# Performance work log

Measured on AMD Instinct MI355X. Metric: run time of the kernel, lower is better.

## Reference

```python
import jax, jax.numpy as jnp
import numpy as np

B, S, D, H = 2, 2048, 1024, 16
HD = D // H          # head_dim = 64
HALF = HD // 2       # rotary pair count = 32


def rope_freqs(seq_len, half, base=10000.0):
    # Llama-style: theta_j = base^(-2j/head_dim), angle m*theta_j
    inv = 1.0 / (base ** (np.arange(0, half, dtype=np.float32) / half))
    ang = np.arange(seq_len, dtype=np.float32)[:, None] * inv[None, :]  # [S, half]
    return jnp.asarray(np.cos(ang)), jnp.asarray(np.sin(ang))


def setup_inputs() -> dict:
    key = jax.random.key(0)
    kx, kq, kk, kv, ko = jax.random.split(key, 5)
    cos, sin = rope_freqs(S, HALF)  # real/imag of m_theta_polar_tensor
    s = 0.02
    return {
        "x": jax.random.normal(kx, (B, S, D), dtype=jnp.float32),
        "freqs_cos": cos,
        "freqs_sin": sin,
        "Wq": jax.random.normal(kq, (D, D), dtype=jnp.float32) * s,
        "Wk": jax.random.normal(kk, (D, D), dtype=jnp.float32) * s,
        "Wv": jax.random.normal(kv, (D, D), dtype=jnp.float32) * s,
        "Wout": jax.random.normal(ko, (D, D), dtype=jnp.float32) * s,
    }


def _apply_rope(t, cos, sin):
    # t: [B, S, H, HD]; rotate consecutive pairs (complex multiply)
    b, s, h, hd = t.shape
    tr = t.reshape(b, s, h, hd // 2, 2)
    t0, t1 = tr[..., 0], tr[..., 1]
    c = cos[None, :, None, :]  # [1, S, 1, HALF]
    sn = sin[None, :, None, :]
    o0 = t0 * c - t1 * sn
    o1 = t0 * sn + t1 * c
    return jnp.stack([o0, o1], axis=-1).reshape(b, s, h, hd)


def reference(x, freqs_cos, freqs_sin, Wq, Wk, Wv, Wout):
    b, s, _ = x.shape
    q = (x @ Wq).reshape(b, s, H, HD)
    k = (x @ Wk).reshape(b, s, H, HD)
    v = (x @ Wv).reshape(b, s, H, HD)
    q = _apply_rope(q, freqs_cos, freqs_sin)
    k = _apply_rope(k, freqs_cos, freqs_sin)
    # [B, H, S, S]
    scores = jnp.einsum("bqhd,bkhd->bhqk", q, k) / jnp.sqrt(jnp.float32(HD))
    causal = jnp.triu(jnp.ones((s, s), dtype=bool), k=1)
    scores = jnp.where(causal[None, None], -jnp.inf, scores)
    weights = jax.nn.softmax(scores, axis=-1)
    vectors = jnp.einsum("bhqk,bkhd->bqhd", weights, v).reshape(b, s, D)
    return vectors @ Wout
```

## Files before the change

kernel.cpp:

```cpp
#include <hip/hip_runtime.h>
#include <stdint.h>

typedef unsigned short u16;
typedef __attribute__((ext_vector_type(8))) short short8;
typedef __attribute__((ext_vector_type(4))) float f32x4;
typedef __attribute__((ext_vector_type(4))) unsigned short ushort4v;
typedef __attribute__((ext_vector_type(2))) unsigned int uint2v;

#define NB 2
#define NS 2048
#define ND 1024
#define NH 16
#define HDIM 64
#define NHALF 32
#define QSCALE 0.18033688f
#define NEGBIG -3.0e38f

__device__ __forceinline__ float bf2f(u16 u) {
  union { unsigned u; float f; } v; v.u = ((unsigned)u) << 16; return v.f;
}
__device__ __forceinline__ u16 f2bf(float f) {
  union { float f; unsigned u; } v; v.f = f;
  unsigned r = v.u + 0x7fffu + ((v.u >> 16) & 1u);
  return (u16)(r >> 16);
}

__device__ __forceinline__ unsigned cvt_pk_bf16(float lo, float hi) {
  unsigned r;
  asm("v_cvt_pk_bf16_f32 %0, %1, %2" : "=v"(r) : "v"(lo), "v"(hi));
  return r;
}

__device__ __forceinline__ void gld_lds16(const u16* g, u16* l) {
  void* gv = (void*)g;
  __builtin_amdgcn_global_load_lds((__attribute__((address_space(1))) void*)gv,
                                   (__attribute__((address_space(3))) void*)l, 16, 0, 0);
}

__global__ void prep(const float* __restrict__ x, u16* __restrict__ xb,
                     const float* __restrict__ W0, const float* __restrict__ W1,
                     const float* __restrict__ W2, const float* __restrict__ W3,
                     u16* __restrict__ dqkv, u16* __restrict__ dout) {
  __shared__ float tile[32][33];
  const int bid = blockIdx.x;
  if (bid < 4096) {
    int i = bid * 256 + threadIdx.x;
    float4 v = ((const float4*)x)[i];
    ushort4v o;
    o.x = f2bf(v.x); o.y = f2bf(v.y); o.z = f2bf(v.z); o.w = f2bf(v.w);
    ((ushort4v*)xb)[i] = o;
  } else {
    int idx = bid - 4096;
    const int z = idx >> 10;
    idx &= 1023;
    const int bx = idx & 31, by = idx >> 5;
    const float* W = (z == 0) ? W0 : (z == 1) ? W1 : (z == 2) ? W2 : W3;
    u16* dst = (z < 3) ? (dqkv + (size_t)z * ND * ND) : dout;
    const int n0 = bx * 32, k0 = by * 32;
    const int tx = threadIdx.x & 31, ty = threadIdx.x >> 5;
#pragma unroll
    for (int i = 0; i < 4; ++i)
      tile[ty + i * 8][tx] = W[(size_t)(k0 + ty + i * 8) * ND + n0 + tx];
    __syncthreads();
#pragma unroll
    for (int i = 0; i < 4; ++i)
      dst[(size_t)(n0 + ty + i * 8) * ND + k0 + tx] = f2bf(tile[tx][ty + i * 8]);
  }
}

template<int MI, int MODE>
__device__ __forceinline__ void gemm_body(
    u16* smem0, int bx, int by,
    const u16* __restrict__ A, const u16* __restrict__ BT,
    u16* __restrict__ qo, u16* __restrict__ ko, u16* __restrict__ vo,
    float* __restrict__ fo,
    const float* __restrict__ cosT, const float* __restrict__ sinT) {
  constexpr int BUFSZ = MI * 2048 + 8192;
  const int tid = threadIdx.x;
  const int w = tid >> 6, lane = tid & 63;
  const int lr = lane & 15, lg = lane >> 4;
  const int bm = by * (MI * 32), bn = bx << 7;
  const int wr = (w >> 1) * (MI * 16), wc = (w & 1) << 6;
  f32x4 acc[MI][4] = {};

  const int arow = tid >> 3;
  const int aslot = (tid & 7) ^ (arow & 7);
  const u16* ags = A + (size_t)(bm + arow) * ND + (aslot << 3);
  const u16* bgs = BT + (size_t)(bn + arow) * ND + (aslot << 3);

  int af_off[MI][2], bf_off[4][2];
#pragma unroll
  for (int mi = 0; mi < MI; ++mi)
#pragma unroll
    for (int kk = 0; kk < 2; ++kk)
      af_off[mi][kk] = (wr + mi * 16 + lr) * 64 + ((((kk << 2) + lg) ^ (lr & 7)) << 3);
#pragma unroll
  for (int ni = 0; ni < 4; ++ni)
#pragma unroll
    for (int kk = 0; kk < 2; ++kk)
      bf_off[ni][kk] = (wc + ni * 16 + lr) * 64 + ((((kk << 2) + lg) ^ (lr & 7)) << 3);

  auto stage = [&](int buf, int kt) {
    u16* dst = smem0 + buf * BUFSZ;
#pragma unroll
    for (int it = 0; it < MI; ++it)
      gld_lds16(ags + it * (32 * ND) + kt, dst + it * 2048 + w * 512);
#pragma unroll
    for (int it = 0; it < 4; ++it)
      gld_lds16(bgs + it * (32 * ND) + kt, dst + MI * 2048 + it * 2048 + w * 512);
  };

  stage(0, 0);
  __syncthreads();
  int cur = 0;
  for (int kt = 0; kt < ND; kt += 64) {
    if (kt + 64 < ND) stage(cur ^ 1, kt + 64);
    const u16* As = smem0 + cur * BUFSZ;
    const u16* Bs = As + MI * 2048;
#pragma unroll
    for (int kk = 0; kk < 2; ++kk) {
      short8 af[MI], bfr[4];
#pragma unroll
      for (int mi = 0; mi < MI; ++mi)
        af[mi] = *(const short8*)(As + af_off[mi][kk]);
#pragma unroll
      for (int ni = 0; ni < 4; ++ni)
        bfr[ni] = *(const short8*)(Bs + bf_off[ni][kk]);
#pragma unroll
      for (int mi = 0; mi < MI; ++mi)
#pragma unroll
        for (int ni = 0; ni < 4; ++ni) {
          if (MODE == 0)
            acc[mi][ni] = __builtin_amdgcn_mfma_f32_16x16x32_bf16(bfr[ni], af[mi], acc[mi][ni], 0, 0, 0);
          else
            acc[mi][ni] = __builtin_amdgcn_mfma_f32_16x16x32_bf16(af[mi], bfr[ni], acc[mi][ni], 0, 0, 0);
        }
    }
    __syncthreads();
    cur ^= 1;
  }

  if (MODE == 0) {
#pragma unroll
    for (int mi = 0; mi < MI; ++mi) {
      const int m = bm + wr + mi * 16 + lr;
      const int b = m >> 11, s = m & 2047;
      const float* cbase = cosT + s * NHALF;
      const float* sbase = sinT + s * NHALF;
#pragma unroll
      for (int ni = 0; ni < 4; ++ni) {
        const int n = bn + wc + ni * 16 + (lg << 2);
        const int which = n >> 10, hh = (n >> 6) & 15, d0 = n & 63;
        u16* dst = which == 0 ? qo : ko;
        const float sc = which == 0 ? QSCALE : 1.0f;
        const float2 cp = *(const float2*)(cbase + (d0 >> 1));
        const float2 sp = *(const float2*)(sbase + (d0 >> 1));
        const float v0 = acc[mi][ni][0], v1 = acc[mi][ni][1];
        const float v2 = acc[mi][ni][2], v3 = acc[mi][ni][3];
        uint2v pk;
        pk.x = cvt_pk_bf16((v0 * cp.x - v1 * sp.x) * sc, (v0 * sp.x + v1 * cp.x) * sc);
        pk.y = cvt_pk_bf16((v2 * cp.y - v3 * sp.y) * sc, (v2 * sp.y + v3 * cp.y) * sc);
        *(uint2v*)(dst + (((size_t)(b * NH + hh) * NS + s) << 6) + d0) = pk;
      }
    }
  } else if (MODE == 1) {
#pragma unroll
    for (int mi = 0; mi < MI; ++mi) {
#pragma unroll
      for (int ni = 0; ni < 4; ++ni) {
        const int n = bn + wc + ni * 16 + lr;
        const int hh = n >> 6, d = n & 63;
        const int m0 = bm + wr + mi * 16 + (lg << 2);
        const int b = m0 >> 11, s0 = m0 & 2047;
        uint2v pk;
        pk.x = cvt_pk_bf16(acc[mi][ni][0], acc[mi][ni][1]);
        pk.y = cvt_pk_bf16(acc[mi][ni][2], acc[mi][ni][3]);
        *(uint2v*)(vo + ((size_t)(b * NH + hh) * HDIM + d) * NS + s0) = pk;
      }
    }
  } else {
#pragma unroll
    for (int mi = 0; mi < MI; ++mi)
#pragma unroll
      for (int ni = 0; ni < 4; ++ni)
#pragma unroll
        for (int j = 0; j < 4; ++j) {
          const int m = bm + wr + mi * 16 + (lg << 2) + j;
          const int n = bn + wc + ni * 16 + lr;
          fo[(size_t)m * ND + n] = acc[mi][ni][j];
        }
  }
}

__global__ __launch_bounds__(256) void gemm_qkv(
    const u16* __restrict__ xb, const u16* __restrict__ WTqkv, const u16* __restrict__ WTv,
    u16* __restrict__ Qb, u16* __restrict__ Kb, u16* __restrict__ VT,
    const float* __restrict__ fc, const float* __restrict__ fs) {
  __shared__ u16 smem[2 * 16384];
  const int bid = blockIdx.x;
  if (bid < 512) {
    gemm_body<4, 0>(smem, bid & 15, bid >> 4, xb, WTqkv, Qb, Kb, nullptr, nullptr, fc, fs);
  } else {
    const int idx = bid - 512;
    gemm_body<2, 1>(smem, idx & 7, idx >> 3, xb, WTv, nullptr, nullptr, VT, nullptr, nullptr, nullptr);
  }
}

__global__ __launch_bounds__(256) void gemm_out_k(
    const u16* __restrict__ Ob, const u16* __restrict__ WTo, float* __restrict__ out) {
  __shared__ u16 smem[2 * 12288];
  gemm_body<2, 2>(smem, blockIdx.x, blockIdx.y, Ob, WTo, nullptr, nullptr, nullptr, out, nullptr, nullptr);
}

__global__ __launch_bounds__(512) void attn_k(
    const u16* __restrict__ Qb, const u16* __restrict__ Kb,
    const u16* __restrict__ VT, u16* __restrict__ Ob) {
  __shared__ u16 K2[2][4096];
  __shared__ u16 V2[2][4096];
  __shared__ u16 Pl[8][1024];
  const int tid = threadIdx.x, w = tid >> 6, lane = tid & 63;
  const int lr = lane & 15, lg = lane >> 4;
  const int bid = blockIdx.x;
  const int xcd = bid & 7, i = bid >> 3;
  const int bh = xcd * 4 + (i & 3);
  const int pair = i >> 2;
  const int b = bh >> 4, h = bh & 15;
  const u16* Qp = Qb + (size_t)bh * NS * HDIM;
  const u16* Kp = Kb + (size_t)bh * NS * HDIM;
  const u16* Vp = VT + (size_t)bh * NS * HDIM;

  int kf_off[4][2], vb_off[4][2], pw_off[4], pa_off[2];
#pragma unroll
  for (int u = 0; u < 4; ++u) {
    const int kvr = (u << 4) + lr;
#pragma unroll
    for (int c = 0; c < 2; ++c)
      kf_off[u][c] = kvr * 64 + ((((c << 6) + (lg << 4)) ^ ((kvr & 7) << 4)) >> 1);
  }
#pragma unroll
  for (int dn = 0; dn < 4; ++dn) {
    const int d = (dn << 4) + lr;
#pragma unroll
    for (int ks = 0; ks < 2; ++ks)
      vb_off[dn][ks] = d * 64 + ((((ks << 6) + (lg << 4)) ^ ((d & 7) << 4)) >> 1);
  }
#pragma unroll
  for (int u = 0; u < 4; ++u)
    pw_off[u] = lr * 64 + ((((u << 5) + (lg << 3)) ^ ((lr & 7) << 4)) >> 1);
#pragma unroll
  for (int ks = 0; ks < 2; ++ks)
    pa_off[ks] = lr * 64 + ((((ks << 6) + (lg << 4)) ^ ((lr & 7) << 4)) >> 1);
  u16* Pw = &Pl[w][0];

  const int rr = tid >> 3, slot = tid & 7;
  const int soff = ((slot ^ (rr & 7)) << 3);
  const u16* kg0 = Kp + (size_t)rr * HDIM + soff;
  const u16* vg0 = Vp + (size_t)rr * NS + soff;

#define STAGE(BUFI, KV0)                                   \
  {                                                        \
    gld_lds16(kg0 + (size_t)(KV0) * HDIM, &K2[BUFI][w * 512]); \
    gld_lds16(vg0 + (KV0),                &V2[BUFI][w * 512]); \
  }

#define STEP(BUF, KVT)                                                            \
  {                                                                               \
    const int kv0 = (KVT) << 6;                                                   \
    if ((KVT) + 1 < nst) STAGE(BUF ^ 1, kv0 + 64);                                \
    const u16* Kl = K2[BUF];                                                      \
    const u16* Vl = V2[BUF];                                                      \
    f32x4 st[4] = {};                                                             \
    __builtin_amdgcn_s_setprio(1);                                                \
    _Pragma("unroll") for (int u = 0; u < 4; ++u)                                 \
      _Pragma("unroll") for (int c = 0; c < 2; ++c)                               \
        st[u] = __builtin_amdgcn_mfma_f32_16x16x32_bf16(                          \
            *(const short8*)(Kl + kf_off[u][c]), qf[c], st[u], 0, 0, 0);          \
    __builtin_amdgcn_s_setprio(0);                                                \
    if (kv0 + 63 > qw) {                                                          \
      _Pragma("unroll") for (int u = 0; u < 4; ++u)                               \
        _Pragma("unroll") for (int j = 0; j < 4; ++j) {                           \
          const int kvg = kv0 + (u << 4) + (lg << 2) + j;                         \
          if (kvg > q_col) st[u][j] = NEGBIG;                                     \
        }                                                                         \
    }                                                                             \
    _Pragma("unroll") for (int u = 0; u < 4; ++u) {                               \
      const float e0 = __builtin_amdgcn_exp2f(st[u][0]);                          \
      const float e1 = __builtin_amdgcn_exp2f(st[u][1]);                          \
      const float e2 = __builtin_amdgcn_exp2f(st[u][2]);                          \
      const float e3 = __builtin_amdgcn_exp2f(st[u][3]);                          \
      lacc += (e0 + e1) + (e2 + e3);                                              \
      uint2v pk;                                                                  \
      pk.x = cvt_pk_bf16(e0, e1);                                                 \
      pk.y = cvt_pk_bf16(e2, e3);                                                 \
      *(uint2v*)(Pw + pw_off[u]) = pk;                                            \
    }                                                                             \
    {                                                                             \
      short8 pa0 = *(const short8*)(Pw + pa_off[0]);                              \
      short8 pa1 = *(const short8*)(Pw + pa_off[1]);                              \
      __builtin_amdgcn_s_setprio(1);                                              \
      _Pragma("unroll") for (int dn = 0; dn < 4; ++dn) {                          \
        o[dn] = __builtin_amdgcn_mfma_f32_16x16x32_bf16(                          \
            pa0, *(const short8*)(Vl + vb_off[dn][0]), o[dn], 0, 0, 0);           \
        o[dn] = __builtin_amdgcn_mfma_f32_16x16x32_bf16(                          \
            pa1, *(const short8*)(Vl + vb_off[dn][1]), o[dn], 0, 0, 0);           \
      }                                                                           \
      __builtin_amdgcn_s_setprio(0);                                              \
    }                                                                             \
    __syncthreads();                                                              \
  }

  for (int seg = 0; seg < 2; ++seg) {
    const int tile = seg ? pair : 15 - pair;
    const int q0 = tile << 7;
    const int qw = q0 + w * 16;
    const int q_col = qw + lr;
    const int nst = 2 * tile + 2;

    short8 qf[2];
#pragma unroll
    for (int c = 0; c < 2; ++c)
      qf[c] = *(const short8*)(Qp + (size_t)(qw + lr) * HDIM + c * 32 + lg * 8);

    f32x4 o[4] = {};
    float lacc = 0.f;

    STAGE(0, 0);
    __syncthreads();

    for (int kvt = 0; kvt < nst; kvt += 2) {
      STEP(0, kvt);
      STEP(1, kvt + 1);
    }

    float rs = lacc;
    rs += __shfl_xor(rs, 16);
    rs += __shfl_xor(rs, 32);
    float li[4];
#pragma unroll
    for (int j = 0; j < 4; ++j) li[j] = 1.0f / __shfl(rs, (lg << 2) + j);
#pragma unroll
    for (int dn = 0; dn < 4; ++dn)
#pragma unroll
      for (int j = 0; j < 4; ++j) {
        const int m = b * NS + qw + (lg << 2) + j;
        const int col = h * 64 + dn * 16 + lr;
        Ob[(size_t)m * ND + col] = f2bf(o[dn][j] * li[j]);
      }
  }
}

extern "C" void kernel_launch(void* const* d_in, const int* in_sizes, int n_in,
                              void* d_out, int out_size, void* d_ws, size_t ws_size,
                              hipStream_t stream) {
  const float* x  = (const float*)d_in[0];
  const float* fc = (const float*)d_in[1];
  const float* fs = (const float*)d_in[2];
  const float* Wq = (const float*)d_in[3];
  const float* Wk = (const float*)d_in[4];
  const float* Wv = (const float*)d_in[5];
  const float* Wo = (const float*)d_in[6];
  float* out = (float*)d_out;
  char* ws = (char*)d_ws;

  u16* xb    = (u16*)(ws);
  u16* Ob    = (u16*)(ws);
  u16* WTqkv = (u16*)(ws + (size_t)(8u << 20));
  u16* WTo   = (u16*)(ws + (size_t)(14u << 20));
  u16* Qb    = (u16*)(ws + (size_t)(16u << 20));
  u16* Kb    = (u16*)(ws + (size_t)(24u << 20));
  u16* VT    = (u16*)(ws + (size_t)(32u << 20));
  u16* WTv   = WTqkv + (size_t)2 * ND * ND;

  prep<<<8192, 256, 0, stream>>>(x, xb, Wq, Wk, Wv, Wo, WTqkv, WTo);
  gemm_qkv<<<1024, 256, 0, stream>>>(xb, WTqkv, WTv, Qb, Kb, VT, fc, fs);
  attn_k<<<256, 512, 0, stream>>>(Qb, Kb, VT, Ob);
  gemm_out_k<<<dim3(8, 64), 256, 0, stream>>>(Ob, WTo, out);
}
```

Baseline: 101.9 us.

## Use 64-row query tiles with 128-wide KV tiles in attention kernel

The attention kernel now uses 4 waves per block (64 query rows) instead of 8 waves (128 rows) and launches twice as many blocks. Each pipeline step consumes a 128-key K/V tile instead of 64, with wider swizzled LDS layouts and a tail step for odd tile counts. The intent is finer causal load balancing across more blocks and fewer barriers per key, at the cost of doubled LDS per block, more registers for the score tiles, and more masked work on the diagonal tile.

```diff
diff --git a/kernel.cpp b/kernel.cpp
--- a/kernel.cpp
+++ b/kernel.cpp
@@ -212,12 +212,12 @@
   gemm_body<2, 2>(smem, blockIdx.x, blockIdx.y, Ob, WTo, nullptr, nullptr, nullptr, out, nullptr, nullptr);
 }
 
-__global__ __launch_bounds__(512) void attn_k(
+__global__ __launch_bounds__(256) void attn_k(
     const u16* __restrict__ Qb, const u16* __restrict__ Kb,
     const u16* __restrict__ VT, u16* __restrict__ Ob) {
-  __shared__ u16 K2[2][4096];
-  __shared__ u16 V2[2][4096];
-  __shared__ u16 Pl[8][1024];
+  __shared__ u16 K2[2][8192];
+  __shared__ u16 V2[2][8192];
+  __shared__ u16 Pl[4][2048];
   const int tid = threadIdx.x, w = tid >> 6, lane = tid & 63;
   const int lr = lane & 15, lg = lane >> 4;
   const int bid = blockIdx.x;
@@ -229,9 +229,9 @@
   const u16* Kp = Kb + (size_t)bh * NS * HDIM;
   const u16* Vp = VT + (size_t)bh * NS * HDIM;
 
-  int kf_off[4][2], vb_off[4][2], pw_off[4], pa_off[2];
-#pragma unroll
-  for (int u = 0; u < 4; ++u) {
+  int kf_off[8][2], vb_off[4][4], pw_off[8], pa_off[4];
+#pragma unroll
+  for (int u = 0; u < 8; ++u) {
     const int kvr = (u << 4) + lr;
 #pragma unroll
     for (int c = 0; c < 2; ++c)
@@ -241,49 +241,54 @@
   for (int dn = 0; dn < 4; ++dn) {
     const int d = (dn << 4) + lr;
 #pragma unroll
-    for (int ks = 0; ks < 2; ++ks)
-      vb_off[dn][ks] = d * 64 + ((((ks << 6) + (lg << 4)) ^ ((d & 7) << 4)) >> 1);
-  }
-#pragma unroll
-  for (int u = 0; u < 4; ++u)
-    pw_off[u] = lr * 64 + ((((u << 5) + (lg << 3)) ^ ((lr & 7) << 4)) >> 1);
-#pragma unroll
-  for (int ks = 0; ks < 2; ++ks)
-    pa_off[ks] = lr * 64 + ((((ks << 6) + (lg << 4)) ^ ((lr & 7) << 4)) >> 1);
+    for (int ks = 0; ks < 4; ++ks)
+      vb_off[dn][ks] = d * 128 + ((((ks << 6) + (lg << 4)) ^ ((d & 15) << 4)) >> 1);
+  }
+#pragma unroll
+  for (int u = 0; u < 8; ++u)
+    pw_off[u] = lr * 128 + ((((u << 5) + (lg << 3)) ^ ((lr & 15) << 4)) >> 1);
+#pragma unroll
+  for (int ks = 0; ks < 4; ++ks)
+    pa_off[ks] = lr * 128 + ((((ks << 6) + (lg << 4)) ^ ((lr & 15) << 4)) >> 1);
   u16* Pw = &Pl[w][0];
 
   const int rr = tid >> 3, slot = tid & 7;
-  const int soff = ((slot ^ (rr & 7)) << 3);
-  const u16* kg0 = Kp + (size_t)rr * HDIM + soff;
-  const u16* vg0 = Vp + (size_t)rr * NS + soff;
-
-#define STAGE(BUFI, KV0)                                   \
-  {                                                        \
-    gld_lds16(kg0 + (size_t)(KV0) * HDIM, &K2[BUFI][w * 512]); \
-    gld_lds16(vg0 + (KV0),                &V2[BUFI][w * 512]); \
+  const int ksoff = ((slot ^ (rr & 7)) << 3);
+  const u16* kg = Kp + (size_t)rr * HDIM + ksoff;
+  const int vr = tid >> 4, vslot = tid & 15;
+  const int vsoff = ((vslot ^ vr) << 3);
+  const u16* vg = Vp + (size_t)vr * NS + vsoff;
+
+#define STAGE(BUFI, KV0)                                                            \
+  {                                                                                 \
+    _Pragma("unroll")                                                               \
+    for (int c = 0; c < 4; ++c) {                                                   \
+      gld_lds16(kg + (size_t)((KV0) + c * 32) * HDIM, &K2[BUFI][c * 2048 + w * 512]); \
+      gld_lds16(vg + (size_t)(c * 16) * NS + (KV0),   &V2[BUFI][c * 2048 + w * 512]); \
+    }                                                                               \
   }
 
 #define STEP(BUF, KVT)                                                            \
   {                                                                               \
-    const int kv0 = (KVT) << 6;                                                   \
-    if ((KVT) + 1 < nst) STAGE(BUF ^ 1, kv0 + 64);                                \
+    const int kv0 = (KVT) << 7;                                                   \
+    if ((KVT) + 1 < nst) STAGE(BUF ^ 1, kv0 + 128);                               \
     const u16* Kl = K2[BUF];                                                      \
     const u16* Vl = V2[BUF];                                                      \
-    f32x4 st[4] = {};                                                             \
+    f32x4 st[8] = {};                                                             \
     __builtin_amdgcn_s_setprio(1);                                                \
-    _Pragma("unroll") for (int u = 0; u < 4; ++u)                                 \
+    _Pragma("unroll") for (int u = 0; u < 8; ++u)                                 \
       _Pragma("unroll") for (int c = 0; c < 2; ++c)                               \
         st[u] = __builtin_amdgcn_mfma_f32_16x16x32_bf16(                          \
             *(const short8*)(Kl + kf_off[u][c]), qf[c], st[u], 0, 0, 0);          \
     __builtin_amdgcn_s_setprio(0);                                                \
-    if (kv0 + 63 > qw) {                                                          \
-      _Pragma("unroll") for (int u = 0; u < 4; ++u)                               \
+    if (kv0 + 127 > qw) {                                                         \
+      _Pragma("unroll") for (int u = 0; u < 8; ++u)                               \
         _Pragma("unroll") for (int j = 0; j < 4; ++j) {                           \
           const int kvg = kv0 + (u << 4) + (lg << 2) + j;                         \
           if (kvg > q_col) st[u][j] = NEGBIG;                                     \
         }                                                                         \
     }                                                                             \
-    _Pragma("unroll") for (int u = 0; u < 4; ++u) {                               \
+    _Pragma("unroll") for (int u = 0; u < 8; ++u) {                               \
       const float e0 = __builtin_amdgcn_exp2f(st[u][0]);                          \
       const float e1 = __builtin_amdgcn_exp2f(st[u][1]);                          \
       const float e2 = __builtin_amdgcn_exp2f(st[u][2]);                          \
@@ -295,26 +300,25 @@
       *(uint2v*)(Pw + pw_off[u]) = pk;                                            \
     }                                                                             \
     {                                                                             \
-      short8 pa0 = *(const short8*)(Pw + pa_off[0]);                              \
-      short8 pa1 = *(const short8*)(Pw + pa_off[1]);                              \
+      short8 pa[4];                                                               \
+      _Pragma("unroll") for (int ks = 0; ks < 4; ++ks)                            \
+        pa[ks] = *(const short8*)(Pw + pa_off[ks]);                               \
       __builtin_amdgcn_s_setprio(1);                                              \
-      _Pragma("unroll") for (int dn = 0; dn < 4; ++dn) {                          \
-        o[dn] = __builtin_amdgcn_mfma_f32_16x16x32_bf16(                          \
-            pa0, *(const short8*)(Vl + vb_off[dn][0]), o[dn], 0, 0, 0);           \
-        o[dn] = __builtin_amdgcn_mfma_f32_16x16x32_bf16(                          \
-            pa1, *(const short8*)(Vl + vb_off[dn][1]), o[dn], 0, 0, 0);           \
-      }                                                                           \
+      _Pragma("unroll") for (int dn = 0; dn < 4; ++dn)                            \
+        _Pragma("unroll") for (int ks = 0; ks < 4; ++ks)                          \
+          o[dn] = __builtin_amdgcn_mfma_f32_16x16x32_bf16(                        \
+              pa[ks], *(const short8*)(Vl + vb_off[dn][ks]), o[dn], 0, 0, 0);     \
       __builtin_amdgcn_s_setprio(0);                                              \
     }                                                                             \
     __syncthreads();                                                              \
   }
 
   for (int seg = 0; seg < 2; ++seg) {
-    const int tile = seg ? pair : 15 - pair;
-    const int q0 = tile << 7;
+    const int tile = seg ? pair : 31 - pair;
+    const int q0 = tile << 6;
     const int qw = q0 + w * 16;
     const int q_col = qw + lr;
-    const int nst = 2 * tile + 2;
+    const int nst = (tile + 2) >> 1;
 
     short8 qf[2];
 #pragma unroll
@@ -327,10 +331,12 @@
     STAGE(0, 0);
     __syncthreads();
 
-    for (int kvt = 0; kvt < nst; kvt += 2) {
+    int kvt = 0;
+    for (; kvt + 2 <= nst; kvt += 2) {
       STEP(0, kvt);
       STEP(1, kvt + 1);
     }
+    if (kvt < nst) STEP(0, kvt);
 
     float rs = lacc;
     rs += __shfl_xor(rs, 16);
@@ -373,6 +379,6 @@
 
   prep<<<8192, 256, 0, stream>>>(x, xb, Wq, Wk, Wv, Wo, WTqkv, WTo);
   gemm_qkv<<<1024, 256, 0, stream>>>(xb, WTqkv, WTv, Qb, Kb, VT, fc, fs);
-  attn_k<<<256, 512, 0, stream>>>(Qb, Kb, VT, Ob);
+  attn_k<<<512, 256, 0, stream>>>(Qb, Kb, VT, Ob);
   gemm_out_k<<<dim3(8, 64), 256, 0, stream>>>(Ob, WTo, out);
 }
```

New measurement: 100.0 us. Within noise of the previous version (-1.8%).
